# Optimization experiments

Measured on AMD Instinct MI355X. Metric: run time of the kernel, lower is better.

## Reference

```python
import jax, jax.numpy as jnp
import numpy as np

FACTOR = 3
N_HEADS = 8


def prob_attention(q, k, v, key):
    # q,k,v: [B, L, H, D]  (Informer ProbAttention, mask_flag falsy, scale=None)
    B, L_Q, H, D = q.shape
    L_K = k.shape[1]
    Q = jnp.swapaxes(q, 1, 2)  # [B,H,L_Q,D]
    K = jnp.swapaxes(k, 1, 2)
    V = jnp.swapaxes(v, 1, 2)
    U_part = min(FACTOR * int(np.ceil(np.log(L_K))), L_K)  # sampled keys per query
    u = min(FACTOR * int(np.ceil(np.log(L_Q))), L_Q)       # active (top) queries
    idx = jax.random.randint(key, (L_Q, U_part), 0, L_K)   # shared across B,H like torch.randint
    K_sample = K[:, :, idx, :]                              # [B,H,L_Q,U_part,D] gather
    QK_sample = jnp.einsum('bhld,bhlsd->bhls', Q, K_sample)
    M = QK_sample.max(axis=-1) - QK_sample.sum(axis=-1) / L_K  # sparsity measure
    _, top_idx = jax.lax.top_k(M, u)                        # [B,H,u]
    Q_reduce = jnp.take_along_axis(Q, top_idx[..., None], axis=2)  # [B,H,u,D]
    scale = 1.0 / np.sqrt(D)
    scores = jnp.einsum('bhud,bhkd->bhuk', Q_reduce, K) * scale     # [B,H,u,L_K]
    attn = jax.nn.softmax(scores, axis=-1)
    out_top = jnp.einsum('bhuk,bhkd->bhud', attn, V)
    # initial context: mean of V over keys, broadcast to every query position
    context = jnp.broadcast_to(V.mean(axis=2, keepdims=True), (B, H, L_Q, D))
    bi = jnp.arange(B)[:, None, None]
    hi = jnp.arange(H)[None, :, None]
    context = context.at[bi, hi, top_idx].set(out_top)
    return jnp.swapaxes(context, 1, 2)  # [B,L_Q,H,D]


def attention_layer(xq, xk, xv, wq, bq, wk, bk, wv, bv, wo, bo, key):
    B, Lq, dm = xq.shape
    Lk = xk.shape[1]
    dk = dm // N_HEADS
    q = (xq @ wq + bq).reshape(B, Lq, N_HEADS, dk)
    k = (xk @ wk + bk).reshape(B, Lk, N_HEADS, dk)
    v = (xv @ wv + bv).reshape(B, Lk, N_HEADS, dk)
    out = prob_attention(q, k, v, key).reshape(B, Lq, dm)
    return out @ wo + bo


def setup_inputs() -> dict:
    key = jax.random.key(0)
    ks = jax.random.split(key, 20)
    B, Ld, Lp, dm = 4, 4096, 4096, 512
    inp = {
        'xs': jax.random.normal(ks[0], (B, Ld + Lp, dm), jnp.float32),
        'xd': jax.random.normal(ks[1], (B, Ld, dm), jnp.float32),
        'xp': jax.random.normal(ks[2], (B, Lp, dm), jnp.float32),
    }
    names = ['w0q', 'w0k', 'w0v', 'w0o', 'b0q', 'b0k', 'b0v', 'b0o',
             'w1q', 'w1k', 'w1v', 'w1o', 'b1q', 'b1k', 'b1v', 'b1o']
    for i, n in enumerate(names):
        if n.startswith('w'):
            inp[n] = jax.random.normal(ks[3 + i], (dm, dm), jnp.float32) * 0.02
        else:
            inp[n] = jnp.zeros((dm,), jnp.float32)
    return inp


def reference(xs, xd, xp,
              w0q, w0k, w0v, w0o, b0q, b0k, b0v, b0o,
              w1q, w1k, w1v, w1o, b1q, b1k, b1v, b1o):
    # dropout layers are identity in eval mode
    xp2 = attention_layer(xp, xd, xd, w0q, b0q, w0k, b0k, w0v, b0v, w0o, b0o,
                          jax.random.key(42))
    xd2 = attention_layer(xd, xp2, xp2, w1q, b1q, w1k, b1k, w1v, b1v, w1o, b1o,
                          jax.random.key(43))
    return xs + jnp.concatenate([xd2, xp2], axis=1)
```

## Files before the change

kernel.cpp:

```cpp
#include <hip/hip_runtime.h>
#include <math.h>

#define NB 4
#define SEQ 4096
#define DM 512
#define NH 8
#define HD 64
#define UU 27
#define NIDX (SEQ*UU)
#define NC 32
#define CS 128
#define PSTRIDE 66
#define LDP 40

typedef unsigned int u32;
typedef unsigned short u16;
typedef __attribute__((ext_vector_type(8))) short short8;
typedef __attribute__((ext_vector_type(4))) short short4v;
typedef __attribute__((ext_vector_type(4))) float f32x4;

__host__ __device__ inline u32 rotl32(u32 x, u32 r){ return (x<<r)|(x>>(32u-r)); }

__host__ __device__ inline void threefry2x32(u32 k0, u32 k1, u32 x0, u32 x1, u32* o0, u32* o1)
{
  u32 ks[3] = { k0, k1, k0 ^ k1 ^ 0x1BD11BDAu };
  x0 += ks[0]; x1 += ks[1];
  const u32 rotA[4] = {13u,15u,26u,6u};
  const u32 rotB[4] = {17u,29u,16u,24u};
  for (int i = 0; i < 5; i++) {
    const u32* rot = (i & 1) ? rotB : rotA;
    for (int j = 0; j < 4; j++) { x0 += x1; x1 = rotl32(x1, rot[j]); x1 ^= x0; }
    x0 += ks[(i+1)%3];
    x1 += ks[(i+2)%3] + (u32)(i+1);
  }
  *o0 = x0; *o1 = x1;
}

__global__ __launch_bounds__(256) void gen_idx_kernel(u32 k2a, u32 k2b, int* __restrict__ idx)
{
  int i = blockIdx.x * 256 + threadIdx.x;
  if (i >= NIDX) return;
  u32 o0, o1;
  threefry2x32(k2a, k2b, 0u, (u32)i, &o0, &o1);
  idx[i] = (int)((o0 ^ o1) & (SEQ - 1));
}

__device__ inline u16 f2bf_rne(float f) {
  u32 u = __float_as_uint(f);
  return (u16)((u + 0x7fffu + ((u >> 16) & 1u)) >> 16);
}
__device__ inline void f2bf_split(float f, u16& hi, u16& lo) {
  u32 u = __float_as_uint(f);
  u16 h = (u16)(u >> 16);
  float hf = __uint_as_float(((u32)h) << 16);
  hi = h;
  lo = f2bf_rne(f - hf);
}

__global__ __launch_bounds__(256) void conv_split(const float* __restrict__ X,
                                                  u16* __restrict__ hi, u16* __restrict__ lo)
{
  long g = (long)blockIdx.x * 256 + threadIdx.x;
  float4 x0 = ((const float4*)X)[g * 2];
  float4 x1 = ((const float4*)X)[g * 2 + 1];
  union { short8 v; u16 s[8]; } h, l;
  float xv[8] = { x0.x, x0.y, x0.z, x0.w, x1.x, x1.y, x1.z, x1.w };
  #pragma unroll
  for (int e = 0; e < 8; e++) f2bf_split(xv[e], h.s[e], l.s[e]);
  ((short8*)hi)[g] = h.v;
  ((short8*)lo)[g]  = l.v;
}

struct WPtrs { const float* w[8]; };
__global__ __launch_bounds__(256) void convw_kernel(WPtrs wp, u16* __restrict__ outp)
{
  const int n  = blockIdx.x;
  const int wi = blockIdx.y;
  const float* W = wp.w[wi];
  u16* hi = outp + (long)wi * 524288 + n * DM;
  u16* lo = hi + 262144;
  for (int k = threadIdx.x; k < DM; k += 256) {
    u16 h, l;
    f2bf_split(W[(long)k * DM + n], h, l);
    hi[k] = h; lo[k] = l;
  }
}

template<int SPLIT>
__global__ __launch_bounds__(256) void gemm_bf(
    const u16* __restrict__ Ah, const u16* __restrict__ Al,
    const u16* __restrict__ Wh, const u16* __restrict__ Wl,
    const float* __restrict__ bias, float* __restrict__ C,
    const float* __restrict__ resid, int rowJump)
{
  __shared__ short As_hi[128 * LDP];
  __shared__ short Ws_hi[128 * LDP];
  __shared__ short As_lo[SPLIT ? 128 * LDP : 8];
  __shared__ short Ws_lo[SPLIT ? 128 * LDP : 8];

  const int t  = threadIdx.x;
  const int rb = blockIdx.x * 128;
  const int cb = blockIdx.y * 128;

  const int r0 = t >> 2, sg = (t & 3) * 8;
  const u16* pAh0 = Ah + (long)(rb + r0) * DM + sg;
  const u16* pAh1 = pAh0 + (long)64 * DM;
  const u16* pWh0 = Wh + (long)(cb + r0) * DM + sg;
  const u16* pWh1 = pWh0 + (long)64 * DM;
  const u16* pAl0 = SPLIT ? (Al + (long)(rb + r0) * DM + sg) : pAh0;
  const u16* pAl1 = pAl0 + (long)64 * DM;
  const u16* pWl0 = SPLIT ? (Wl + (long)(cb + r0) * DM + sg) : pWh0;
  const u16* pWl1 = pWl0 + (long)64 * DM;

  short* dA0 = &As_hi[r0 * LDP + sg];
  short* dA1 = &As_hi[(r0 + 64) * LDP + sg];
  short* dW0 = &Ws_hi[r0 * LDP + sg];
  short* dW1 = &Ws_hi[(r0 + 64) * LDP + sg];
  short* dAl0 = &As_lo[SPLIT ? r0 * LDP + sg : 0];
  short* dAl1 = &As_lo[SPLIT ? (r0 + 64) * LDP + sg : 0];
  short* dWl0 = &Ws_lo[SPLIT ? r0 * LDP + sg : 0];
  short* dWl1 = &Ws_lo[SPLIT ? (r0 + 64) * LDP + sg : 0];

  const int lane = t & 63, wv = t >> 6;
  const int wm = (wv & 1) * 64, wn = (wv >> 1) * 64;
  const int fr = lane & 15, fq = lane >> 4;

  f32x4 acc[4][4];
  #pragma unroll
  for (int i = 0; i < 4; i++)
    #pragma unroll
    for (int j = 0; j < 4; j++) acc[i][j] = (f32x4)(0.f);

  for (int k0 = 0; k0 < DM; k0 += 32) {
    short8 va0 = *(const short8*)(pAh0 + k0);
    short8 va1 = *(const short8*)(pAh1 + k0);
    short8 vw0 = *(const short8*)(pWh0 + k0);
    short8 vw1 = *(const short8*)(pWh1 + k0);
    short8 la0, la1, lw0, lw1;
    if (SPLIT) {
      la0 = *(const short8*)(pAl0 + k0);
      la1 = *(const short8*)(pAl1 + k0);
      lw0 = *(const short8*)(pWl0 + k0);
      lw1 = *(const short8*)(pWl1 + k0);
    }

    __syncthreads();

    *(short8*)dA0 = va0; *(short8*)dA1 = va1;
    *(short8*)dW0 = vw0; *(short8*)dW1 = vw1;
    if (SPLIT) {
      *(short8*)dAl0 = la0; *(short8*)dAl1 = la1;
      *(short8*)dWl0 = lw0; *(short8*)dWl1 = lw1;
    }
    __syncthreads();

    short8 a_hi[4], b_hi[4];
    #pragma unroll
    for (int i = 0; i < 4; i++)
      a_hi[i] = *(const short8*)&As_hi[(wm + i * 16 + fr) * LDP + fq * 8];
    #pragma unroll
    for (int j = 0; j < 4; j++)
      b_hi[j] = *(const short8*)&Ws_hi[(wn + j * 16 + fr) * LDP + fq * 8];
    #pragma unroll
    for (int i = 0; i < 4; i++)
      #pragma unroll
      for (int j = 0; j < 4; j++)
        acc[i][j] = __builtin_amdgcn_mfma_f32_16x16x32_bf16(a_hi[i], b_hi[j], acc[i][j], 0, 0, 0);
    if (SPLIT) {
      short8 a_lo[4], b_lo[4];
      #pragma unroll
      for (int i = 0; i < 4; i++)
        a_lo[i] = *(const short8*)&As_lo[(wm + i * 16 + fr) * LDP + fq * 8];
      #pragma unroll
      for (int j = 0; j < 4; j++)
        b_lo[j] = *(const short8*)&Ws_lo[(wn + j * 16 + fr) * LDP + fq * 8];
      #pragma unroll
      for (int i = 0; i < 4; i++)
        #pragma unroll
        for (int j = 0; j < 4; j++) {
          acc[i][j] = __builtin_amdgcn_mfma_f32_16x16x32_bf16(a_hi[i], b_lo[j], acc[i][j], 0, 0, 0);
          acc[i][j] = __builtin_amdgcn_mfma_f32_16x16x32_bf16(a_lo[i], b_hi[j], acc[i][j], 0, 0, 0);
        }
    }
  }

  #pragma unroll
  for (int j = 0; j < 4; j++) {
    int col = cb + wn + j * 16 + fr;
    float bv = bias[col];
    #pragma unroll
    for (int i = 0; i < 4; i++) {
      int row0 = rb + wm + i * 16 + fq * 4;
      #pragma unroll
      for (int r = 0; r < 4; r++) {
        int row = row0 + r;
        long off = (long)row * DM + (long)(row >> 12) * rowJump + col;
        float v = acc[i][j][r] + bv;
        if (resid) v += resid[off];
        C[off] = v;
      }
    }
  }
}

__global__ __launch_bounds__(256) void mscore_kernel(const float* __restrict__ Q, const float* __restrict__ K,
                                                     const int* __restrict__ idx, float* __restrict__ M)
{
  const int wl = threadIdx.x >> 6, lane = threadIdx.x & 63;
  const int bl = blockIdx.x * 4 + wl;
  const int b = bl >> 12, l = bl & (SEQ - 1);

  const float4* qp = (const float4*)(Q + (long)bl * DM + lane * 8);
  float4 q0 = qp[0], q1 = qp[1];

  const int* ip = idx + l * UU;
  int idxv = ip[lane < UU ? lane : 0];
  int chv = idxv >> 9;

  const float* kb = K + ((long)b << 12) * DM + lane * 8;
  float mx = -INFINITY, sm = 0.f;
  #pragma unroll 1
  for (int c = 0; c < 8; c++) {
    unsigned long long msk = __ballot(chv == c) & ((1ull << UU) - 1ull);
    while (msk) {
      int s = __builtin_ctzll(msk);
      msk &= msk - 1;
      int kl = __shfl(idxv, s, 64);
      const float4* kp = (const float4*)(kb + (long)kl * DM);
      float4 k0 = kp[0], k1 = kp[1];
      float dot;
      dot = q0.x * k0.x;
      dot = fmaf(q0.y, k0.y, dot); dot = fmaf(q0.z, k0.z, dot); dot = fmaf(q0.w, k0.w, dot);
      dot = fmaf(q1.x, k1.x, dot); dot = fmaf(q1.y, k1.y, dot);
      dot = fmaf(q1.z, k1.z, dot); dot = fmaf(q1.w, k1.w, dot);
      dot += __shfl_xor(dot, 1, 64);
      dot += __shfl_xor(dot, 2, 64);
      dot += __shfl_xor(dot, 4, 64);
      mx = fmaxf(mx, dot);
      sm += dot;
    }
  }
  if ((lane & 7) == 0) {
    int h = lane >> 3;
    M[(((long)b * NH + h) << 12) + l] = mx - sm * (1.0f / (float)SEQ);
  }
}

__global__ __launch_bounds__(256) void topk_kernel(const float* __restrict__ M, int* __restrict__ topidx)
{
  __shared__ float vals[SEQ];
  __shared__ float rv[256];
  __shared__ int   ri[256];
  const float* m = M + (long)blockIdx.x * SEQ;
  for (int i = threadIdx.x; i < SEQ; i += 256) vals[i] = m[i];
  __syncthreads();
  for (int it = 0; it < UU; it++) {
    float bv = -INFINITY; int bi = 0x7fffffff;
    for (int i = threadIdx.x; i < SEQ; i += 256) {
      float v = vals[i];
      if (v > bv) { bv = v; bi = i; }
    }
    rv[threadIdx.x] = bv; ri[threadIdx.x] = bi;
    __syncthreads();
    for (int s = 128; s > 0; s >>= 1) {
      if (threadIdx.x < s) {
        float ov = rv[threadIdx.x + s]; int oi = ri[threadIdx.x + s];
        if (ov > rv[threadIdx.x] || (ov == rv[threadIdx.x] && oi < ri[threadIdx.x])) {
          rv[threadIdx.x] = ov; ri[threadIdx.x] = oi;
        }
      }
      __syncthreads();
    }
    if (threadIdx.x == 0) { topidx[blockIdx.x * UU + it] = ri[0]; vals[ri[0]] = -INFINITY; }
    __syncthreads();
  }
}

__global__ __launch_bounds__(512) void vmean_partial(const float* __restrict__ V, float* __restrict__ vsum)
{
  int b = blockIdx.x >> 5, chunk = blockIdx.x & 31;
  int c = threadIdx.x;
  const float* p = V + ((long)b * SEQ + chunk * 128) * DM + c;
  float s = 0.f;
  for (int l = 0; l < 128; l++) s += p[(long)l * DM];
  atomicAdd(&vsum[b * DM + c], s);
}

__global__ __launch_bounds__(256) void attn_part(const float* __restrict__ Q, const float* __restrict__ K,
                                                 const float* __restrict__ V, const int* __restrict__ topidx,
                                                 float* __restrict__ partial)
{
  __shared__ float Qs[UU][HD];
  __shared__ float S[UU][CS];
  __shared__ float Vt[CS][HD];
  __shared__ float m_s[UU], l_s[UU];

  const int t = threadIdx.x;
  const int bh = blockIdx.x;
  const int chunk = blockIdx.y;
  const int b = bh >> 3, h = bh & 7;
  const long kbase = ((long)(b << 12) + chunk * CS) * DM + h * HD;
  const int* tp = topidx + bh * UU;

  for (int i = t; i < UU * HD; i += 256) {
    int u = i >> 6, d = i & 63;
    Qs[u][d] = Q[((long)(b << 12) + tp[u]) * DM + h * HD + d];
  }
  for (int i = t; i < CS * (HD / 4); i += 256) {
    int row = i >> 4, c4 = (i & 15) << 2;
    *(float4*)&Vt[row][c4] = *(const float4*)(V + kbase + (long)row * DM + c4);
  }
  __syncthreads();

  {
    const int l = t >> 1, half = t & 1, d0 = half * 32;
    const float* kp = K + kbase + (long)l * DM + d0;
    float4 kr[8];
    #pragma unroll
    for (int j = 0; j < 8; j++) kr[j] = *(const float4*)(kp + j * 4);
    #pragma unroll 1
    for (int u = 0; u < UU; u++) {
      const float4* qf = (const float4*)&Qs[u][d0];
      float dot = 0.f;
      #pragma unroll
      for (int j = 0; j < 8; j++) {
        float4 q = qf[j];
        dot = fmaf(q.x, kr[j].x, dot); dot = fmaf(q.y, kr[j].y, dot);
        dot = fmaf(q.z, kr[j].z, dot); dot = fmaf(q.w, kr[j].w, dot);
      }
      float tot = dot + __shfl_xor(dot, 1, 64);
      if (half == 0) S[u][l] = tot * 0.125f;
    }
  }
  __syncthreads();

  {
    const int u = t >> 3, il = t & 7;
    if (u < UU) {
      float mx = -INFINITY;
      for (int l = il; l < CS; l += 8) mx = fmaxf(mx, S[u][l]);
      #pragma unroll
      for (int m = 1; m < 8; m <<= 1) mx = fmaxf(mx, __shfl_xor(mx, m, 64));
      float ps = 0.f;
      for (int l = il; l < CS; l += 8) {
        float e = expf(S[u][l] - mx);
        S[u][l] = e;
        ps += e;
      }
      #pragma unroll
      for (int m = 1; m < 8; m <<= 1) ps += __shfl_xor(ps, m, 64);
      if (il == 0) { m_s[u] = mx; l_s[u] = ps; }
    }
  }
  __syncthreads();

  {
    const int d = t & 63, g = t >> 6;
    for (int u = g; u < UU; u += 4) {
      float acc = 0.f;
      #pragma unroll 4
      for (int l = 0; l < CS; l += 4) {
        float4 p4 = *(const float4*)&S[u][l];
        acc = fmaf(p4.x, Vt[l][d],     acc);
        acc = fmaf(p4.y, Vt[l + 1][d], acc);
        acc = fmaf(p4.z, Vt[l + 2][d], acc);
        acc = fmaf(p4.w, Vt[l + 3][d], acc);
      }
      float* pp = partial + (((long)bh * NC + chunk) * UU + u) * PSTRIDE;
      pp[2 + d] = acc;
      if (d == 0) { pp[0] = m_s[u]; pp[1] = l_s[u]; }
    }
  }
}

__global__ __launch_bounds__(64) void attn_merge_bf(const float* __restrict__ partial, const int* __restrict__ topidx,
                                                    u16* __restrict__ hi, u16* __restrict__ lo)
{
  int g = blockIdx.x;
  int bh = g / UU, u = g % UU;
  int b = bh >> 3, h = bh & 7;
  int d = threadIdx.x;
  float M = -INFINITY, S = 0.f, acc = 0.f;
  for (int c = 0; c < NC; c++) {
    const float* pp = partial + (((long)bh * NC + c) * UU + u) * PSTRIDE;
    float mc = pp[0], sc = pp[1], a = pp[2 + d];
    if (mc > M) {
      float r = expf(M - mc);
      acc *= r; S *= r; M = mc;
    }
    float w = expf(mc - M);
    acc = fmaf(a, w, acc);
    S = fmaf(sc, w, S);
  }
  int ql = topidx[g];
  long o = ((long)(b << 12) + ql) * DM + h * HD + d;
  u16 hv, lv;
  f2bf_split(acc / S, hv, lv);
  hi[o] = hv; lo[o] = lv;
}

__global__ __launch_bounds__(256) void ctx_fill_bf(const float* __restrict__ vsum,
                                                   u16* __restrict__ hi, u16* __restrict__ lo)
{
  long g = (long)blockIdx.x * 256 + threadIdx.x;
  int b = (int)(g >> 19);
  int c4 = (int)(g & 127);
  float4 v = ((const float4*)vsum)[b * 128 + c4];
  const float s = 1.0f / (float)SEQ;
  float xv[4] = { v.x * s, v.y * s, v.z * s, v.w * s };
  union { short4v v; u16 s[4]; } h, l;
  #pragma unroll
  for (int e = 0; e < 4; e++) f2bf_split(xv[e], h.s[e], l.s[e]);
  ((short4v*)hi)[g] = h.v;
  ((short4v*)lo)[g]  = l.v;
}

__global__ __launch_bounds__(256) void add_upper(const float* __restrict__ xs, const float* __restrict__ xp2,
                                                 float* __restrict__ out)
{
  long g = (long)blockIdx.x * 256 + threadIdx.x;
  int b = (int)(g >> 19);
  long rem = g & 524287;
  float4 p = ((const float4*)xp2)[g];
  long o = ((long)b * 8192 + SEQ) * 128 + rem;
  float4 x = ((const float4*)xs)[o];
  x.x += p.x; x.y += p.y; x.z += p.z; x.w += p.w;
  ((float4*)out)[o] = x;
}

extern "C" void kernel_launch(void* const* d_in, const int* in_sizes, int n_in,
                              void* d_out, int out_size, void* d_ws, size_t ws_size,
                              hipStream_t stream)
{
  const float* xs  = (const float*)d_in[0];
  const float* xd  = (const float*)d_in[1];
  const float* xp  = (const float*)d_in[2];
  const float* w0q = (const float*)d_in[3];
  const float* w0k = (const float*)d_in[4];
  const float* w0v = (const float*)d_in[5];
  const float* w0o = (const float*)d_in[6];
  const float* b0q = (const float*)d_in[7];
  const float* b0k = (const float*)d_in[8];
  const float* b0v = (const float*)d_in[9];
  const float* b0o = (const float*)d_in[10];
  const float* w1q = (const float*)d_in[11];
  const float* w1k = (const float*)d_in[12];
  const float* w1v = (const float*)d_in[13];
  const float* w1o = (const float*)d_in[14];
  const float* b1q = (const float*)d_in[15];
  const float* b1k = (const float*)d_in[16];
  const float* b1v = (const float*)d_in[17];
  const float* b1o = (const float*)d_in[18];
  float* out = (float*)d_out;

  const long BIG = (long)NB * SEQ * DM;
  float* A  = (float*)d_ws;
  float* Bb = A  + BIG;
  float* Cc = Bb + BIG;
  float* Dd = Cc + BIG;
  float* ex = Dd + BIG;
  float* Pq  = ex + BIG;
  float* Pkv = Pq + BIG;

  int*   idxbuf = (int*)ex;
  float* Mbuf   = ex + NIDX;
  int*   topidx = (int*)(Mbuf + (long)NB * NH * SEQ);
  float* vsum   = (float*)(topidx + NB * NH * UU);
  u16*   wpl    = (u16*)(ex + (1 << 20));

  u16* Pq_hi  = (u16*)Pq;   u16* Pq_lo  = Pq_hi  + BIG;
  u16* Pkv_hi = (u16*)Pkv;  u16* Pkv_lo = Pkv_hi + BIG;
  auto whi = [&](int i){ return wpl + (long)i * 524288; };
  auto wlo = [&](int i){ return wpl + (long)i * 524288 + 262144; };

  dim3 gg(128, 4);
  dim3 ag(NB * NH, NC);
  u32 k2a, k2b;

  WPtrs wp;
  wp.w[0] = w0q; wp.w[1] = w0k; wp.w[2] = w0v; wp.w[3] = w0o;
  wp.w[4] = w1q; wp.w[5] = w1k; wp.w[6] = w1v; wp.w[7] = w1o;
  convw_kernel<<<dim3(512, 8), 256, 0, stream>>>(wp, wpl);

  threefry2x32(0u, 42u, 0u, 1u, &k2a, &k2b);
  gen_idx_kernel<<<(NIDX + 255) / 256, 256, 0, stream>>>(k2a, k2b, idxbuf);
  conv_split<<<4096, 256, 0, stream>>>(xp, Pq_hi, Pq_lo);
  conv_split<<<4096, 256, 0, stream>>>(xd, Pkv_hi, Pkv_lo);
  gemm_bf<1><<<gg, 256, 0, stream>>>(Pq_hi,  Pq_lo,  whi(0), wlo(0), b0q, A,  nullptr, 0);
  gemm_bf<1><<<gg, 256, 0, stream>>>(Pkv_hi, Pkv_lo, whi(1), wlo(1), b0k, Bb, nullptr, 0);
  gemm_bf<1><<<gg, 256, 0, stream>>>(Pkv_hi, Pkv_lo, whi(2), wlo(2), b0v, Cc, nullptr, 0);
  mscore_kernel<<<NB * SEQ / 4, 256, 0, stream>>>(A, Bb, idxbuf, Mbuf);
  topk_kernel<<<NB * NH, 256, 0, stream>>>(Mbuf, topidx);
  hipMemsetAsync(vsum, 0, NB * DM * sizeof(float), stream);
  vmean_partial<<<NB * 32, 512, 0, stream>>>(Cc, vsum);
  attn_part<<<ag, 256, 0, stream>>>(A, Bb, Cc, topidx, Dd);
  ctx_fill_bf<<<8192, 256, 0, stream>>>(vsum, Pq_hi, Pq_lo);
  attn_merge_bf<<<NB * NH * UU, 64, 0, stream>>>(Dd, topidx, Pq_hi, Pq_lo);
  gemm_bf<1><<<gg, 256, 0, stream>>>(Pq_hi, Pq_lo, whi(3), wlo(3), b0o, Bb, nullptr, 0);
  add_upper<<<8192, 256, 0, stream>>>(xs, Bb, out);

  threefry2x32(0u, 43u, 0u, 1u, &k2a, &k2b);
  gen_idx_kernel<<<(NIDX + 255) / 256, 256, 0, stream>>>(k2a, k2b, idxbuf);
  gemm_bf<1><<<gg, 256, 0, stream>>>(Pkv_hi, Pkv_lo, whi(4), wlo(4), b1q, A, nullptr, 0);
  conv_split<<<4096, 256, 0, stream>>>(Bb, Pq_hi, Pq_lo);
  gemm_bf<1><<<gg, 256, 0, stream>>>(Pq_hi, Pq_lo, whi(5), wlo(5), b1k, Cc, nullptr, 0);
  gemm_bf<1><<<gg, 256, 0, stream>>>(Pq_hi, Pq_lo, whi(6), wlo(6), b1v, Dd, nullptr, 0);
  mscore_kernel<<<NB * SEQ / 4, 256, 0, stream>>>(A, Cc, idxbuf, Mbuf);
  topk_kernel<<<NB * NH, 256, 0, stream>>>(Mbuf, topidx);
  hipMemsetAsync(vsum, 0, NB * DM * sizeof(float), stream);
  vmean_partial<<<NB * 32, 512, 0, stream>>>(Dd, vsum);
  attn_part<<<ag, 256, 0, stream>>>(A, Cc, Dd, topidx, Bb);
  ctx_fill_bf<<<8192, 256, 0, stream>>>(vsum, Pkv_hi, Pkv_lo);
  attn_merge_bf<<<NB * NH * UU, 64, 0, stream>>>(Bb, topidx, Pkv_hi, Pkv_lo);
  gemm_bf<1><<<gg, 256, 0, stream>>>(Pkv_hi, Pkv_lo, whi(7), wlo(7), b1o, out, xs, SEQ * DM);
}
```

Baseline: 863.4 us.

## Double-buffer GEMM with direct global-to-LDS loads and fuse K/V projections

Rewrites the split-bf16 GEMM to stage tiles straight into a swizzled, double-buffered LDS layout with global_load_lds, so the next k-slice loads while MFMAs run on the current one. The weight layout is regrouped so all hi halves are contiguous, then all lo halves. The K and V projections now run as one launch over a 1024-wide output, with the epilogue choosing bias and destination by column. This aims to hide load latency, drop the register round-trip and one barrier per step, and cut launches, at the cost of more LDS and a vmcnt(0) wait each iteration.

After: 833.4 us. 1.04x faster.

```diff
diff --git a/kernel.cpp b/kernel.cpp
--- a/kernel.cpp
+++ b/kernel.cpp
@@ -11,7 +11,6 @@
 #define NC 32
 #define CS 128
 #define PSTRIDE 66
-#define LDP 40
 
 typedef unsigned int u32;
 typedef unsigned short u16;
@@ -77,8 +76,8 @@
   const int n  = blockIdx.x;
   const int wi = blockIdx.y;
   const float* W = wp.w[wi];
-  u16* hi = outp + (long)wi * 524288 + n * DM;
-  u16* lo = hi + 262144;
+  u16* hi = outp + (long)wi * 262144 + n * DM;
+  u16* lo = hi + 8L * 262144;
   for (int k = threadIdx.x; k < DM; k += 256) {
     u16 h, l;
     f2bf_split(W[(long)k * DM + n], h, l);
@@ -86,44 +85,38 @@
   }
 }
 
-template<int SPLIT>
+__device__ inline void gld16(const u16* g, short* l) {
+  __builtin_amdgcn_global_load_lds((const u32*)g, (u32*)l, 16, 0, 0);
+}
+
 __global__ __launch_bounds__(256) void gemm_bf(
     const u16* __restrict__ Ah, const u16* __restrict__ Al,
     const u16* __restrict__ Wh, const u16* __restrict__ Wl,
-    const float* __restrict__ bias, float* __restrict__ C,
+    const float* __restrict__ bias0, const float* __restrict__ bias1,
+    float* __restrict__ C0, float* __restrict__ C1,
     const float* __restrict__ resid, int rowJump)
 {
-  __shared__ short As_hi[128 * LDP];
-  __shared__ short Ws_hi[128 * LDP];
-  __shared__ short As_lo[SPLIT ? 128 * LDP : 8];
-  __shared__ short Ws_lo[SPLIT ? 128 * LDP : 8];
+  __shared__ short LB[2][4][4096];
 
   const int t  = threadIdx.x;
   const int rb = blockIdx.x * 128;
   const int cb = blockIdx.y * 128;
 
-  const int r0 = t >> 2, sg = (t & 3) * 8;
-  const u16* pAh0 = Ah + (long)(rb + r0) * DM + sg;
-  const u16* pAh1 = pAh0 + (long)64 * DM;
-  const u16* pWh0 = Wh + (long)(cb + r0) * DM + sg;
-  const u16* pWh1 = pWh0 + (long)64 * DM;
-  const u16* pAl0 = SPLIT ? (Al + (long)(rb + r0) * DM + sg) : pAh0;
-  const u16* pAl1 = pAl0 + (long)64 * DM;
-  const u16* pWl0 = SPLIT ? (Wl + (long)(cb + r0) * DM + sg) : pWh0;
-  const u16* pWl1 = pWl0 + (long)64 * DM;
-
-  short* dA0 = &As_hi[r0 * LDP + sg];
-  short* dA1 = &As_hi[(r0 + 64) * LDP + sg];
-  short* dW0 = &Ws_hi[r0 * LDP + sg];
-  short* dW1 = &Ws_hi[(r0 + 64) * LDP + sg];
-  short* dAl0 = &As_lo[SPLIT ? r0 * LDP + sg : 0];
-  short* dAl1 = &As_lo[SPLIT ? (r0 + 64) * LDP + sg : 0];
-  short* dWl0 = &Ws_lo[SPLIT ? r0 * LDP + sg : 0];
-  short* dWl1 = &Ws_lo[SPLIT ? (r0 + 64) * LDP + sg : 0];
+  const int slot = (t & 7) ^ ((t >> 3) & 7);
+  const int c8   = slot & 3;
+  const int rloc = ((t >> 3) << 1) + (slot >> 2);
+  const u16* sAh = Ah + (long)(rb + rloc) * DM + c8 * 8;
+  const u16* sWh = Wh + (long)(cb + rloc) * DM + c8 * 8;
+  const u16* sAl = Al + (long)(rb + rloc) * DM + c8 * 8;
+  const u16* sWl = Wl + (long)(cb + rloc) * DM + c8 * 8;
+  const int w512 = (t >> 6) * 512;
 
   const int lane = t & 63, wv = t >> 6;
   const int wm = (wv & 1) * 64, wn = (wv >> 1) * 64;
   const int fr = lane & 15, fq = lane >> 4;
+  const int fsw = (fr >> 1) * 64 + ((((fr & 1) * 4 + fq) ^ (fr >> 1)) * 8);
+  const int a_off = wm * 32 + fsw;
+  const int b_off = wn * 32 + fsw;
 
   f32x4 acc[4][4];
   #pragma unroll
@@ -131,73 +124,67 @@
     #pragma unroll
     for (int j = 0; j < 4; j++) acc[i][j] = (f32x4)(0.f);
 
-  for (int k0 = 0; k0 < DM; k0 += 32) {
-    short8 va0 = *(const short8*)(pAh0 + k0);
-    short8 va1 = *(const short8*)(pAh1 + k0);
-    short8 vw0 = *(const short8*)(pWh0 + k0);
-    short8 vw1 = *(const short8*)(pWh1 + k0);
-    short8 la0, la1, lw0, lw1;
-    if (SPLIT) {
-      la0 = *(const short8*)(pAl0 + k0);
-      la1 = *(const short8*)(pAl1 + k0);
-      lw0 = *(const short8*)(pWl0 + k0);
-      lw1 = *(const short8*)(pWl1 + k0);
-    }
-
+#define STAGE(buf, k0s) do { \
+    gld16(sAh + (k0s),               &LB[buf][0][w512]); \
+    gld16(sAh + (k0s) + 64 * DM,     &LB[buf][0][w512 + 2048]); \
+    gld16(sWh + (k0s),               &LB[buf][1][w512]); \
+    gld16(sWh + (k0s) + 64 * DM,     &LB[buf][1][w512 + 2048]); \
+    gld16(sAl + (k0s),               &LB[buf][2][w512]); \
+    gld16(sAl + (k0s) + 64 * DM,     &LB[buf][2][w512 + 2048]); \
+    gld16(sWl + (k0s),               &LB[buf][3][w512]); \
+    gld16(sWl + (k0s) + 64 * DM,     &LB[buf][3][w512 + 2048]); \
+  } while (0)
+
+  STAGE(0, 0);
+  #pragma unroll 2
+  for (int ks = 0; ks < 16; ks++) {
+    const int cur = ks & 1;
+    asm volatile("s_waitcnt vmcnt(0)" ::: "memory");
     __syncthreads();
-
-    *(short8*)dA0 = va0; *(short8*)dA1 = va1;
-    *(short8*)dW0 = vw0; *(short8*)dW1 = vw1;
-    if (SPLIT) {
-      *(short8*)dAl0 = la0; *(short8*)dAl1 = la1;
-      *(short8*)dWl0 = lw0; *(short8*)dWl1 = lw1;
-    }
-    __syncthreads();
-
-    short8 a_hi[4], b_hi[4];
-    #pragma unroll
-    for (int i = 0; i < 4; i++)
-      a_hi[i] = *(const short8*)&As_hi[(wm + i * 16 + fr) * LDP + fq * 8];
-    #pragma unroll
-    for (int j = 0; j < 4; j++)
-      b_hi[j] = *(const short8*)&Ws_hi[(wn + j * 16 + fr) * LDP + fq * 8];
+    if (ks < 15) STAGE(cur ^ 1, (ks + 1) * 32);
+
+    short8 a_hi[4], b_hi[4], a_lo[4], b_lo[4];
+    #pragma unroll
+    for (int i = 0; i < 4; i++) a_hi[i] = *(const short8*)&LB[cur][0][a_off + i * 512];
+    #pragma unroll
+    for (int j = 0; j < 4; j++) b_hi[j] = *(const short8*)&LB[cur][1][b_off + j * 512];
+    #pragma unroll
+    for (int i = 0; i < 4; i++) a_lo[i] = *(const short8*)&LB[cur][2][a_off + i * 512];
+    #pragma unroll
+    for (int j = 0; j < 4; j++) b_lo[j] = *(const short8*)&LB[cur][3][b_off + j * 512];
+
     #pragma unroll
     for (int i = 0; i < 4; i++)
       #pragma unroll
       for (int j = 0; j < 4; j++)
         acc[i][j] = __builtin_amdgcn_mfma_f32_16x16x32_bf16(a_hi[i], b_hi[j], acc[i][j], 0, 0, 0);
-    if (SPLIT) {
-      short8 a_lo[4], b_lo[4];
+    #pragma unroll
+    for (int i = 0; i < 4; i++)
       #pragma unroll
-      for (int i = 0; i < 4; i++)
-        a_lo[i] = *(const short8*)&As_lo[(wm + i * 16 + fr) * LDP + fq * 8];
-      #pragma unroll
-      for (int j = 0; j < 4; j++)
-        b_lo[j] = *(const short8*)&Ws_lo[(wn + j * 16 + fr) * LDP + fq * 8];
-      #pragma unroll
-      for (int i = 0; i < 4; i++)
-        #pragma unroll
-        for (int j = 0; j < 4; j++) {
-          acc[i][j] = __builtin_amdgcn_mfma_f32_16x16x32_bf16(a_hi[i], b_lo[j], acc[i][j], 0, 0, 0);
-          acc[i][j] = __builtin_amdgcn_mfma_f32_16x16x32_bf16(a_lo[i], b_hi[j], acc[i][j], 0, 0, 0);
-        }
-    }
-  }
+      for (int j = 0; j < 4; j++) {
+        acc[i][j] = __builtin_amdgcn_mfma_f32_16x16x32_bf16(a_hi[i], b_lo[j], acc[i][j], 0, 0, 0);
+        acc[i][j] = __builtin_amdgcn_mfma_f32_16x16x32_bf16(a_lo[i], b_hi[j], acc[i][j], 0, 0, 0);
+      }
+  }
+#undef STAGE
 
   #pragma unroll
   for (int j = 0; j < 4; j++) {
     int col = cb + wn + j * 16 + fr;
-    float bv = bias[col];
+    const float* bp = (col < DM) ? bias0 : bias1;
+    float* Cp = (col < DM) ? C0 : C1;
+    int cc = col & (DM - 1);
+    float bv = bp[cc];
     #pragma unroll
     for (int i = 0; i < 4; i++) {
       int row0 = rb + wm + i * 16 + fq * 4;
       #pragma unroll
       for (int r = 0; r < 4; r++) {
         int row = row0 + r;
-        long off = (long)row * DM + (long)(row >> 12) * rowJump + col;
+        long off = (long)row * DM + (long)(row >> 12) * rowJump + cc;
         float v = acc[i][j][r] + bv;
         if (resid) v += resid[off];
-        C[off] = v;
+        Cp[off] = v;
       }
     }
   }
@@ -470,10 +457,11 @@
 
   u16* Pq_hi  = (u16*)Pq;   u16* Pq_lo  = Pq_hi  + BIG;
   u16* Pkv_hi = (u16*)Pkv;  u16* Pkv_lo = Pkv_hi + BIG;
-  auto whi = [&](int i){ return wpl + (long)i * 524288; };
-  auto wlo = [&](int i){ return wpl + (long)i * 524288 + 262144; };
+  auto whi = [&](int i){ return wpl + (long)i * 262144; };
+  auto wlo = [&](int i){ return wpl + 8L * 262144 + (long)i * 262144; };
 
   dim3 gg(128, 4);
+  dim3 gkv(128, 8);
   dim3 ag(NB * NH, NC);
   u32 k2a, k2b;
 
@@ -486,9 +474,8 @@
   gen_idx_kernel<<<(NIDX + 255) / 256, 256, 0, stream>>>(k2a, k2b, idxbuf);
   conv_split<<<4096, 256, 0, stream>>>(xp, Pq_hi, Pq_lo);
   conv_split<<<4096, 256, 0, stream>>>(xd, Pkv_hi, Pkv_lo);
-  gemm_bf<1><<<gg, 256, 0, stream>>>(Pq_hi,  Pq_lo,  whi(0), wlo(0), b0q, A,  nullptr, 0);
-  gemm_bf<1><<<gg, 256, 0, stream>>>(Pkv_hi, Pkv_lo, whi(1), wlo(1), b0k, Bb, nullptr, 0);
-  gemm_bf<1><<<gg, 256, 0, stream>>>(Pkv_hi, Pkv_lo, whi(2), wlo(2), b0v, Cc, nullptr, 0);
+  gemm_bf<<<gg, 256, 0, stream>>>(Pq_hi,  Pq_lo,  whi(0), wlo(0), b0q, b0q, A,  A,  nullptr, 0);
+  gemm_bf<<<gkv, 256, 0, stream>>>(Pkv_hi, Pkv_lo, whi(1), wlo(1), b0k, b0v, Bb, Cc, nullptr, 0);
   mscore_kernel<<<NB * SEQ / 4, 256, 0, stream>>>(A, Bb, idxbuf, Mbuf);
   topk_kernel<<<NB * NH, 256, 0, stream>>>(Mbuf, topidx);
   hipMemsetAsync(vsum, 0, NB * DM * sizeof(float), stream);
@@ -496,15 +483,14 @@
   attn_part<<<ag, 256, 0, stream>>>(A, Bb, Cc, topidx, Dd);
   ctx_fill_bf<<<8192, 256, 0, stream>>>(vsum, Pq_hi, Pq_lo);
   attn_merge_bf<<<NB * NH * UU, 64, 0, stream>>>(Dd, topidx, Pq_hi, Pq_lo);
-  gemm_bf<1><<<gg, 256, 0, stream>>>(Pq_hi, Pq_lo, whi(3), wlo(3), b0o, Bb, nullptr, 0);
+  gemm_bf<<<gg, 256, 0, stream>>>(Pq_hi, Pq_lo, whi(3), wlo(3), b0o, b0o, Bb, Bb, nullptr, 0);
   add_upper<<<8192, 256, 0, stream>>>(xs, Bb, out);
 
   threefry2x32(0u, 43u, 0u, 1u, &k2a, &k2b);
   gen_idx_kernel<<<(NIDX + 255) / 256, 256, 0, stream>>>(k2a, k2b, idxbuf);
-  gemm_bf<1><<<gg, 256, 0, stream>>>(Pkv_hi, Pkv_lo, whi(4), wlo(4), b1q, A, nullptr, 0);
+  gemm_bf<<<gg, 256, 0, stream>>>(Pkv_hi, Pkv_lo, whi(4), wlo(4), b1q, b1q, A, A, nullptr, 0);
   conv_split<<<4096, 256, 0, stream>>>(Bb, Pq_hi, Pq_lo);
-  gemm_bf<1><<<gg, 256, 0, stream>>>(Pq_hi, Pq_lo, whi(5), wlo(5), b1k, Cc, nullptr, 0);
-  gemm_bf<1><<<gg, 256, 0, stream>>>(Pq_hi, Pq_lo, whi(6), wlo(6), b1v, Dd, nullptr, 0);
+  gemm_bf<<<gkv, 256, 0, stream>>>(Pq_hi, Pq_lo, whi(5), wlo(5), b1k, b1v, Cc, Dd, nullptr, 0);
   mscore_kernel<<<NB * SEQ / 4, 256, 0, stream>>>(A, Cc, idxbuf, Mbuf);
   topk_kernel<<<NB * NH, 256, 0, stream>>>(Mbuf, topidx);
   hipMemsetAsync(vsum, 0, NB * DM * sizeof(float), stream);
@@ -512,5 +498,5 @@
   attn_part<<<ag, 256, 0, stream>>>(A, Cc, Dd, topidx, Bb);
   ctx_fill_bf<<<8192, 256, 0, stream>>>(vsum, Pkv_hi, Pkv_lo);
   attn_merge_bf<<<NB * NH * UU, 64, 0, stream>>>(Bb, topidx, Pkv_hi, Pkv_lo);
-  gemm_bf<1><<<gg, 256, 0, stream>>>(Pkv_hi, Pkv_lo, whi(7), wlo(7), b1o, out, xs, SEQ * DM);
-}
+  gemm_bf<<<gg, 256, 0, stream>>>(Pkv_hi, Pkv_lo, whi(7), wlo(7), b1o, b1o, out, out, xs, SEQ * DM);
+}
```
